# Optimization experiments

Measured on AMD Instinct MI355X. Metric: run time of the kernel, lower is better.

## Reference

```python
import jax, jax.numpy as jnp
import numpy as np

N_NODES = 100000
N_EDGES = 3200000
DIM = 64


def setup_inputs() -> dict:
    key = jax.random.key(0)
    k1, k2, k3, k4, k5, k6 = jax.random.split(key, 6)
    lap_rows = jax.random.randint(k1, (N_EDGES,), 0, N_NODES, dtype=jnp.int32)
    lap_cols = jax.random.randint(k2, (N_EDGES,), 0, N_NODES, dtype=jnp.int32)
    # normalized-Laplacian-like positive values
    lap_vals = jax.random.uniform(k3, (N_EDGES,), dtype=jnp.float32) * 0.1
    features = jax.random.normal(k4, (N_NODES, DIM), dtype=jnp.float32)
    scale = 1.0 / np.sqrt(DIM)
    W1 = jax.random.normal(k5, (DIM, DIM), dtype=jnp.float32) * scale
    b1 = jnp.zeros((DIM,), dtype=jnp.float32)
    W2 = jax.random.normal(k6, (DIM, DIM), dtype=jnp.float32) * scale
    b2 = jnp.zeros((DIM,), dtype=jnp.float32)
    return {
        "lap_rows": lap_rows, "lap_cols": lap_cols, "lap_vals": lap_vals,
        "features": features, "W1": W1, "b1": b1, "W2": W2, "b2": b2,
    }


def reference(lap_rows, lap_cols, lap_vals, features, W1, b1, W2, b2):
    # x = L @ features  (COO SpMM: gather source rows, scale, scatter-add to dest)
    msgs = lap_vals[:, None] * features[lap_cols]            # [E, D]
    x = jax.ops.segment_sum(msgs, lap_rows, num_segments=N_NODES)  # [N, D]
    # output = (L+I) E W1 + (L E * E) W2
    inter_part1 = (features + x) @ W1 + b1                   # [N, D_out]
    inter_part2 = (x * features) @ W2 + b2                   # [N, D_out]
    return inter_part1 + inter_part2
```

## Files before the change

kernel.cpp:

```cpp
#include <hip/hip_runtime.h>
#include <hip/hip_fp16.h>

#define DIM 64
#define RPB 64
#define RPB_SHIFT 6
#define SUP_SHIFT 11
#define SB_MAX 64
#define CAP 4096
#define CAPK (CAP / 1024)
#define HTILE_H 16384
#define HTILE1 8192
#define HTILE2 4096

typedef _Float16 half8 __attribute__((ext_vector_type(8)));
typedef float    f32x4 __attribute__((ext_vector_type(4)));

__global__ __launch_bounds__(256) void scatter_kernel(
    const int* __restrict__ rows, const int* __restrict__ cols,
    const float* __restrict__ vals, const float* __restrict__ feat,
    float* __restrict__ x, int E)
{
    unsigned long long t = (unsigned long long)blockIdx.x * blockDim.x + threadIdx.x;
    int e = (int)(t >> 6);
    int d = (int)(t & 63);
    if (e >= E) return;
    int r = rows[e];
    int c = cols[e];
    float v = vals[e];
    float f = feat[(size_t)c * DIM + d];
    atomicAdd(&x[(size_t)r * DIM + d], v * f);
}

__global__ __launch_bounds__(256) void cvt_kernel(
    const float* __restrict__ f, __half* __restrict__ h, int n2)
{
    int i = blockIdx.x * blockDim.x + threadIdx.x;
    if (i < n2) {
        float2 v = ((const float2*)f)[i];
        __half2 o;
        o.x = __float2half(v.x);
        o.y = __float2half(v.y);
        ((__half2*)h)[i] = o;
    }
}

__global__ __launch_bounds__(1024) void hist_kernel(
    const int* __restrict__ rows, int* __restrict__ gcnt, int E, int B)
{
    extern __shared__ int lcnt[];
    for (int i = threadIdx.x; i < B; i += 1024) lcnt[i] = 0;
    __syncthreads();
    int base = blockIdx.x * HTILE_H;
#pragma unroll
    for (int k = 0; k < HTILE_H / 1024; ++k) {
        int e = base + k * 1024 + threadIdx.x;
        if (e < E) atomicAdd(&lcnt[rows[e] >> RPB_SHIFT], 1);
    }
    __syncthreads();
    for (int i = threadIdx.x; i < B; i += 1024)
        if (lcnt[i]) atomicAdd(&gcnt[i], lcnt[i]);
}

__global__ __launch_bounds__(1024) void scan_kernel(
    const int* __restrict__ gcnt, int* __restrict__ offs, int* __restrict__ cursors,
    int* __restrict__ soffs, int* __restrict__ scursors, int B, int SB, int E)
{
    __shared__ int lds[2048];
    int t = threadIdx.x;
    int c0 = (t < B) ? gcnt[t] : 0;
    int c1 = (t + 1024 < B) ? gcnt[t + 1024] : 0;
    lds[t] = c0;
    lds[t + 1024] = c1;
    __syncthreads();
    for (int off = 1; off < 2048; off <<= 1) {
        int a = (t >= off) ? lds[t - off] : 0;
        int b = lds[t + 1024 - off];
        __syncthreads();
        lds[t] += a;
        lds[t + 1024] += b;
        __syncthreads();
    }
    if (t < B) {
        int e = lds[t] - c0;
        offs[t] = e; cursors[t] = e;
        if ((t & 31) == 0) { soffs[t >> 5] = e; scursors[t >> 5] = e; }
    }
    int t2 = t + 1024;
    if (t2 < B) {
        int e = lds[t2] - c1;
        offs[t2] = e; cursors[t2] = e;
        if ((t2 & 31) == 0) { soffs[t2 >> 5] = e; scursors[t2 >> 5] = e; }
    }
    if (t == 0) { offs[B] = E; soffs[SB] = E; }
}

__global__ __launch_bounds__(1024) void superbin_kernel(
    const int* __restrict__ rows, const int* __restrict__ cols,
    const float* __restrict__ vals, int* __restrict__ scursors,
    unsigned long long* __restrict__ sorted1, int E, int SB)
{
    __shared__ int cnt[SB_MAX];
    __shared__ int bse[SB_MAX];
    const int tid = threadIdx.x;
    if (tid < SB) cnt[tid] = 0;
    __syncthreads();
    const int tbase = blockIdx.x * HTILE1;
    int rr[HTILE1 / 1024];
#pragma unroll
    for (int k = 0; k < HTILE1 / 1024; ++k) {
        int e = tbase + k * 1024 + tid;
        rr[k] = (e < E) ? rows[e] : -1;
        if (rr[k] >= 0) atomicAdd(&cnt[rr[k] >> SUP_SHIFT], 1);
    }
    __syncthreads();
    if (tid < SB) {
        int c = cnt[tid];
        bse[tid] = c ? atomicAdd(&scursors[tid], c) : 0;
        cnt[tid] = 0;
    }
    __syncthreads();
#pragma unroll
    for (int k = 0; k < HTILE1 / 1024; ++k) {
        int e = tbase + k * 1024 + tid;
        if (rr[k] >= 0) {
            int r  = rr[k];
            int sb = r >> SUP_SHIFT;
            int slot = bse[sb] + atomicAdd(&cnt[sb], 1);
            unsigned long long pk =
                ((unsigned long long)__float_as_uint(vals[e]) << 32) |
                ((unsigned long long)(r & 2047) << 17) |
                (unsigned)cols[e];
            sorted1[slot] = pk;
        }
    }
}

__global__ __launch_bounds__(1024) void finebin_kernel(
    const unsigned long long* __restrict__ sorted1, const int* __restrict__ soffs,
    int* __restrict__ cursors, unsigned long long* __restrict__ sorted2,
    int E, int B, int SB)
{
    extern __shared__ int l[];
    int* cnt  = l;
    int* bse  = l + B;
    int* sofl = l + 2 * B;
    const int tid = threadIdx.x;
    if (tid <= SB) sofl[tid] = soffs[tid];
    for (int i = tid; i < B; i += 1024) cnt[i] = 0;
    __syncthreads();

    const int tbase = blockIdx.x * HTILE2;
    int sb0 = 0;
    {
        int lo = 0, hi = SB - 1;
        while (lo < hi) {
            int mid = (lo + hi + 1) >> 1;
            if (sofl[mid] <= tbase) lo = mid; else hi = mid - 1;
        }
        sb0 = lo;
    }

    unsigned long long pkr[HTILE2 / 1024];
    int fidr[HTILE2 / 1024];
#pragma unroll
    for (int k = 0; k < HTILE2 / 1024; ++k) {
        int i = tbase + k * 1024 + tid;
        if (i < E) {
            pkr[k] = sorted1[i];
            int sb = sb0;
            while (sofl[sb + 1] <= i) sb++;
            fidr[k] = (sb << 5) + (int)((pkr[k] >> 23) & 31);
            atomicAdd(&cnt[fidr[k]], 1);
        } else fidr[k] = -1;
    }
    __syncthreads();
    for (int i = tid; i < B; i += 1024) {
        int c = cnt[i];
        bse[i] = c ? atomicAdd(&cursors[i], c) : 0;
    }
    __syncthreads();
    for (int i = tid; i < B; i += 1024) cnt[i] = 0;
    __syncthreads();
#pragma unroll
    for (int k = 0; k < HTILE2 / 1024; ++k) {
        if (fidr[k] >= 0) {
            int f = fidr[k];
            int slot = bse[f] + atomicAdd(&cnt[f], 1);
            sorted2[slot] = pkr[k];
        }
    }
}

__global__ __launch_bounds__(1024, 8) void reduce_fused_mfma_kernel(
    const unsigned long long* __restrict__ sorted, const int* __restrict__ offs,
    const __half* __restrict__ featH,
    const float* __restrict__ W1, const float* __restrict__ b1,
    const float* __restrict__ W2, const float* __restrict__ b2,
    float* __restrict__ out, int N)
{
    __shared__ unsigned long long spk[CAP];
    __shared__ int rcnt[RPB];
    __shared__ int rbase[RPB];
    __shared__ float xs[RPB][DIM + 4];

    const int tid = threadIdx.x;
    const int b   = blockIdx.x;
    const int s    = offs[b];
    const int tend = offs[b + 1];
    int nl = tend - s;
    if (nl > CAP) nl = CAP;

    if (tid < RPB) rcnt[tid] = 0;
    __syncthreads();

    unsigned long long pkreg[CAPK];
#pragma unroll
    for (int k = 0; k < CAPK; ++k) {
        int i = k * 1024 + tid;
        pkreg[k] = (i < nl) ? sorted[s + i] : 0ull;
    }
#pragma unroll
    for (int k = 0; k < CAPK; ++k) {
        int i = k * 1024 + tid;
        if (i < nl) atomicAdd(&rcnt[(int)((pkreg[k] >> 17) & (RPB - 1))], 1);
    }
    __syncthreads();

    if (tid < 64) {
        int c = rcnt[tid];
        int v = c;
#pragma unroll
        for (int off = 1; off < 64; off <<= 1) {
            int u = __shfl_up(v, off, 64);
            if (tid >= off) v += u;
        }
        rbase[tid] = v - c;
        rcnt[tid]  = 0;
    }
    __syncthreads();

#pragma unroll
    for (int k = 0; k < CAPK; ++k) {
        int i = k * 1024 + tid;
        if (i < nl) {
            int rl  = (int)((pkreg[k] >> 17) & (RPB - 1));
            int idx = atomicAdd(&rcnt[rl], 1);
            spk[rbase[rl] + idx] = pkreg[k];
        }
    }
    __syncthreads();

    const int w    = tid >> 6;
    const int lane = tid & 63;
    const int eg   = lane >> 3;
    const int sub  = lane & 7;
    const int rowbase = b * RPB;

#pragma unroll
    for (int j = 0; j < RPB / 16; ++j) {
        int rl = w + 16 * j;
        int rs = rbase[rl];
        int rt = rs + rcnt[rl];

        __half2 hacc[4];
#pragma unroll
        for (int q = 0; q < 4; ++q) hacc[q] = __floats2half2_rn(0.f, 0.f);

        int i = rs + eg;
        for (; i + 24 < rt; i += 32) {
            unsigned long long pk0 = spk[i];
            unsigned long long pk1 = spk[i + 8];
            unsigned long long pk2 = spk[i + 16];
            unsigned long long pk3 = spk[i + 24];
            float4 rw0 = *(const float4*)(featH + (size_t)(pk0 & 0x1FFFFu) * DIM + sub * 8);
            float4 rw1 = *(const float4*)(featH + (size_t)(pk1 & 0x1FFFFu) * DIM + sub * 8);
            float4 rw2 = *(const float4*)(featH + (size_t)(pk2 & 0x1FFFFu) * DIM + sub * 8);
            float4 rw3 = *(const float4*)(featH + (size_t)(pk3 & 0x1FFFFu) * DIM + sub * 8);
            __half2 v0 = __float2half2_rn(__uint_as_float((unsigned)(pk0 >> 32)));
            __half2 v1 = __float2half2_rn(__uint_as_float((unsigned)(pk1 >> 32)));
            __half2 v2 = __float2half2_rn(__uint_as_float((unsigned)(pk2 >> 32)));
            __half2 v3 = __float2half2_rn(__uint_as_float((unsigned)(pk3 >> 32)));
            hacc[0] = __hfma2(v0, __builtin_bit_cast(__half2, rw0.x), hacc[0]);
            hacc[1] = __hfma2(v0, __builtin_bit_cast(__half2, rw0.y), hacc[1]);
            hacc[2] = __hfma2(v0, __builtin_bit_cast(__half2, rw0.z), hacc[2]);
            hacc[3] = __hfma2(v0, __builtin_bit_cast(__half2, rw0.w), hacc[3]);
            hacc[0] = __hfma2(v1, __builtin_bit_cast(__half2, rw1.x), hacc[0]);
            hacc[1] = __hfma2(v1, __builtin_bit_cast(__half2, rw1.y), hacc[1]);
            hacc[2] = __hfma2(v1, __builtin_bit_cast(__half2, rw1.z), hacc[2]);
            hacc[3] = __hfma2(v1, __builtin_bit_cast(__half2, rw1.w), hacc[3]);
            hacc[0] = __hfma2(v2, __builtin_bit_cast(__half2, rw2.x), hacc[0]);
            hacc[1] = __hfma2(v2, __builtin_bit_cast(__half2, rw2.y), hacc[1]);
            hacc[2] = __hfma2(v2, __builtin_bit_cast(__half2, rw2.z), hacc[2]);
            hacc[3] = __hfma2(v2, __builtin_bit_cast(__half2, rw2.w), hacc[3]);
            hacc[0] = __hfma2(v3, __builtin_bit_cast(__half2, rw3.x), hacc[0]);
            hacc[1] = __hfma2(v3, __builtin_bit_cast(__half2, rw3.y), hacc[1]);
            hacc[2] = __hfma2(v3, __builtin_bit_cast(__half2, rw3.z), hacc[2]);
            hacc[3] = __hfma2(v3, __builtin_bit_cast(__half2, rw3.w), hacc[3]);
        }
        for (; i < rt; i += 8) {
            unsigned long long pk0 = spk[i];
            float4 rw0 = *(const float4*)(featH + (size_t)(pk0 & 0x1FFFFu) * DIM + sub * 8);
            __half2 v0 = __float2half2_rn(__uint_as_float((unsigned)(pk0 >> 32)));
            hacc[0] = __hfma2(v0, __builtin_bit_cast(__half2, rw0.x), hacc[0]);
            hacc[1] = __hfma2(v0, __builtin_bit_cast(__half2, rw0.y), hacc[1]);
            hacc[2] = __hfma2(v0, __builtin_bit_cast(__half2, rw0.z), hacc[2]);
            hacc[3] = __hfma2(v0, __builtin_bit_cast(__half2, rw0.w), hacc[3]);
        }

        float acc[8];
#pragma unroll
        for (int q = 0; q < 4; ++q) {
            acc[2 * q]     = __low2float(hacc[q]);
            acc[2 * q + 1] = __high2float(hacc[q]);
        }
#pragma unroll
        for (int off = 8; off < 64; off <<= 1) {
#pragma unroll
            for (int q = 0; q < 8; ++q)
                acc[q] += __shfl_xor(acc[q], off, 64);
        }

        if (eg == 0) {
            float4 o; o.x = acc[0]; o.y = acc[1]; o.z = acc[2]; o.w = acc[3];
            *(float4*)&xs[rl][sub * 8] = o;
        } else if (eg == 1) {
            float4 o; o.x = acc[4]; o.y = acc[5]; o.z = acc[6]; o.w = acc[7];
            *(float4*)&xs[rl][sub * 8 + 4] = o;
        }
    }
    __syncthreads();

    if (tend - s > CAP) {
        for (int e = s + CAP + tid; e < tend; e += 1024) {
            unsigned long long pk = sorted[e];
            int rl = (int)((pk >> 17) & (RPB - 1));
            float v = __uint_as_float((unsigned)(pk >> 32));
            int c = (int)(pk & 0x1FFFFu);
            for (int d = 0; d < DIM; ++d)
                atomicAdd(&xs[rl][d], v * __half2float(featH[(size_t)c * DIM + d]));
        }
        __syncthreads();
    }

    {
        const int m    = lane & 15;
        const int quad = lane >> 4;
        const int tile = w >> 2;
        const int c    = w & 3;

        half8 wf[4];
#pragma unroll
        for (int t = 0; t < 4; ++t) {
            const float* Wsrc = (t < 2) ? W1 : W2;
            int kbase = (t & 1) * 32 + quad * 8;
            half8 wv;
#pragma unroll
            for (int j = 0; j < 8; ++j)
                wv[j] = (_Float16)Wsrc[(kbase + j) * DIM + c * 16 + m];
            wf[t] = wv;
        }
        float bias = b1[c * 16 + m] + b2[c * 16 + m];

        int rowl = tile * 16 + m;
        int grow = rowbase + rowl;
        int rldr = (grow < N) ? grow : (N - 1);
        const __half* fp = featH + (size_t)rldr * DIM + quad * 8;
        half8 flo = *(const half8*)(fp);
        half8 fhi = *(const half8*)(fp + 32);
        const float* xp = &xs[rowl][quad * 8];
        float4 xl0 = *(const float4*)(xp);
        float4 xl1 = *(const float4*)(xp + 4);
        float4 xh0 = *(const float4*)(xp + 32);
        float4 xh1 = *(const float4*)(xp + 36);

        half8 alo, ahi, blo, bhi;
        _Float16 xv;
        xv = (_Float16)xl0.x; alo[0] = flo[0] + xv; blo[0] = flo[0] * xv;
        xv = (_Float16)xl0.y; alo[1] = flo[1] + xv; blo[1] = flo[1] * xv;
        xv = (_Float16)xl0.z; alo[2] = flo[2] + xv; blo[2] = flo[2] * xv;
        xv = (_Float16)xl0.w; alo[3] = flo[3] + xv; blo[3] = flo[3] * xv;
        xv = (_Float16)xl1.x; alo[4] = flo[4] + xv; blo[4] = flo[4] * xv;
        xv = (_Float16)xl1.y; alo[5] = flo[5] + xv; blo[5] = flo[5] * xv;
        xv = (_Float16)xl1.z; alo[6] = flo[6] + xv; blo[6] = flo[6] * xv;
        xv = (_Float16)xl1.w; alo[7] = flo[7] + xv; blo[7] = flo[7] * xv;
        xv = (_Float16)xh0.x; ahi[0] = fhi[0] + xv; bhi[0] = fhi[0] * xv;
        xv = (_Float16)xh0.y; ahi[1] = fhi[1] + xv; bhi[1] = fhi[1] * xv;
        xv = (_Float16)xh0.z; ahi[2] = fhi[2] + xv; bhi[2] = fhi[2] * xv;
        xv = (_Float16)xh0.w; ahi[3] = fhi[3] + xv; bhi[3] = fhi[3] * xv;
        xv = (_Float16)xh1.x; ahi[4] = fhi[4] + xv; bhi[4] = fhi[4] * xv;
        xv = (_Float16)xh1.y; ahi[5] = fhi[5] + xv; bhi[5] = fhi[5] * xv;
        xv = (_Float16)xh1.z; ahi[6] = fhi[6] + xv; bhi[6] = fhi[6] * xv;
        xv = (_Float16)xh1.w; ahi[7] = fhi[7] + xv; bhi[7] = fhi[7] * xv;

        f32x4 a0 = { bias, bias, bias, bias };
        a0 = __builtin_amdgcn_mfma_f32_16x16x32_f16(alo, wf[0], a0, 0, 0, 0);
        a0 = __builtin_amdgcn_mfma_f32_16x16x32_f16(ahi, wf[1], a0, 0, 0, 0);
        a0 = __builtin_amdgcn_mfma_f32_16x16x32_f16(blo, wf[2], a0, 0, 0, 0);
        a0 = __builtin_amdgcn_mfma_f32_16x16x32_f16(bhi, wf[3], a0, 0, 0, 0);

#pragma unroll
        for (int reg = 0; reg < 4; ++reg) {
            int orow = rowbase + tile * 16 + quad * 4 + reg;
            if (orow < N)
                out[(size_t)orow * DIM + c * 16 + m] = a0[reg];
        }
    }
}

__global__ __launch_bounds__(256) void transform_mfma_kernel(
    const __half* __restrict__ featH, const float* __restrict__ x,
    const float* __restrict__ W1, const float* __restrict__ b1,
    const float* __restrict__ W2, const float* __restrict__ b2,
    float* __restrict__ out, int N)
{
    const int lane = threadIdx.x & 63;
    const int m    = lane & 15;
    const int quad = lane >> 4;

    half8 wfrag[4][4];
#pragma unroll
    for (int t = 0; t < 4; ++t) {
        const float* Wsrc = (t < 2) ? W1 : W2;
        int kbase = (t & 1) * 32 + quad * 8;
#pragma unroll
        for (int c = 0; c < 4; ++c) {
            int col = c * 16 + m;
            half8 w;
#pragma unroll
            for (int j = 0; j < 8; ++j)
                w[j] = (_Float16)Wsrc[(kbase + j) * DIM + col];
            wfrag[t][c] = w;
        }
    }
    float bias[4];
#pragma unroll
    for (int c = 0; c < 4; ++c)
        bias[c] = b1[c * 16 + m] + b2[c * 16 + m];

    const int ntiles = (N + 15) / 16;
    const int wid    = (int)((blockIdx.x * blockDim.x + threadIdx.x) >> 6);
    const int nwaves = (int)((gridDim.x * blockDim.x) >> 6);

    for (int tile = wid; tile < ntiles; tile += nwaves) {
        int row  = tile * 16 + m;
        int rldr = (row < N) ? row : (N - 1);
        const __half* fp = featH + (size_t)rldr * DIM + quad * 8;
        const float*  xp = x     + (size_t)rldr * DIM + quad * 8;
        half8 flo = *(const half8*)(fp);
        half8 fhi = *(const half8*)(fp + 32);
        float4 xl0 = *(const float4*)(xp);
        float4 xl1 = *(const float4*)(xp + 4);
        float4 xh0 = *(const float4*)(xp + 32);
        float4 xh1 = *(const float4*)(xp + 36);

        half8 alo, ahi, blo, bhi;
        _Float16 xv;
        xv = (_Float16)xl0.x; alo[0] = flo[0] + xv; blo[0] = flo[0] * xv;
        xv = (_Float16)xl0.y; alo[1] = flo[1] + xv; blo[1] = flo[1] * xv;
        xv = (_Float16)xl0.z; alo[2] = flo[2] + xv; blo[2] = flo[2] * xv;
        xv = (_Float16)xl0.w; alo[3] = flo[3] + xv; blo[3] = flo[3] * xv;
        xv = (_Float16)xl1.x; alo[4] = flo[4] + xv; blo[4] = flo[4] * xv;
        xv = (_Float16)xl1.y; alo[5] = flo[5] + xv; blo[5] = flo[5] * xv;
        xv = (_Float16)xl1.z; alo[6] = flo[6] + xv; blo[6] = flo[6] * xv;
        xv = (_Float16)xl1.w; alo[7] = flo[7] + xv; blo[7] = flo[7] * xv;
        xv = (_Float16)xh0.x; ahi[0] = fhi[0] + xv; bhi[0] = fhi[0] * xv;
        xv = (_Float16)xh0.y; ahi[1] = fhi[1] + xv; bhi[1] = fhi[1] * xv;
        xv = (_Float16)xh0.z; ahi[2] = fhi[2] + xv; bhi[2] = fhi[2] * xv;
        xv = (_Float16)xh0.w; ahi[3] = fhi[3] + xv; bhi[3] = fhi[3] * xv;
        xv = (_Float16)xh1.x; ahi[4] = fhi[4] + xv; bhi[4] = fhi[4] * xv;
        xv = (_Float16)xh1.y; ahi[5] = fhi[5] + xv; bhi[5] = fhi[5] * xv;
        xv = (_Float16)xh1.z; ahi[6] = fhi[6] + xv; bhi[6] = fhi[6] * xv;
        xv = (_Float16)xh1.w; ahi[7] = fhi[7] + xv; bhi[7] = fhi[7] * xv;

        f32x4 acc[4];
#pragma unroll
        for (int c = 0; c < 4; ++c) {
            f32x4 a0 = { bias[c], bias[c], bias[c], bias[c] };
            a0 = __builtin_amdgcn_mfma_f32_16x16x32_f16(alo, wfrag[0][c], a0, 0, 0, 0);
            a0 = __builtin_amdgcn_mfma_f32_16x16x32_f16(ahi, wfrag[1][c], a0, 0, 0, 0);
            a0 = __builtin_amdgcn_mfma_f32_16x16x32_f16(blo, wfrag[2][c], a0, 0, 0, 0);
            a0 = __builtin_amdgcn_mfma_f32_16x16x32_f16(bhi, wfrag[3][c], a0, 0, 0, 0);
            acc[c] = a0;
        }

#pragma unroll
        for (int reg = 0; reg < 4; ++reg) {
            int orow = tile * 16 + quad * 4 + reg;
            if (orow < N) {
#pragma unroll
                for (int c = 0; c < 4; ++c)
                    out[(size_t)orow * DIM + c * 16 + m] = acc[c][reg];
            }
        }
    }
}

extern "C" void kernel_launch(void* const* d_in, const int* in_sizes, int n_in,
                              void* d_out, int out_size, void* d_ws, size_t ws_size,
                              hipStream_t stream)
{
    const int*   rows = (const int*)d_in[0];
    const int*   cols = (const int*)d_in[1];
    const float* vals = (const float*)d_in[2];
    const float* feat = (const float*)d_in[3];
    const float* W1   = (const float*)d_in[4];
    const float* b1   = (const float*)d_in[5];
    const float* W2   = (const float*)d_in[6];
    const float* b2   = (const float*)d_in[7];
    float* out = (float*)d_out;

    const int E  = in_sizes[0];
    const int N  = in_sizes[3] / DIM;
    const int B  = (N + RPB - 1) / RPB;
    const int SB = (B + 31) / 32;

    char* ws = (char*)d_ws;
    size_t xBytes     = (size_t)N * DIM * sizeof(float);
    size_t hBytes     = (((size_t)N * DIM * sizeof(__half)) + 255) / 256 * 256;
    size_t offsBytes  = (((size_t)(B + 1) * sizeof(int)) + 255) / 256 * 256;
    size_t cursBytes  = (((size_t)B * sizeof(int)) + 255) / 256 * 256;
    size_t soffBytes  = (((size_t)(SB + 1) * sizeof(int)) + 255) / 256 * 256;
    size_t scurBytes  = (((size_t)SB * sizeof(int)) + 255) / 256 * 256;
    size_t sortBytes  = (size_t)E * 8;

    float*              x        = (float*)ws;
    __half*             featH    = (__half*)(ws + xBytes);
    int*                offs     = (int*)(ws + xBytes + hBytes);
    int*                cursors  = (int*)(ws + xBytes + hBytes + offsBytes);
    int*                soffs    = (int*)(ws + xBytes + hBytes + offsBytes + cursBytes);
    int*                scursors = (int*)(ws + xBytes + hBytes + offsBytes + cursBytes + soffBytes);
    unsigned long long* sorted1  = (unsigned long long*)(ws + xBytes + hBytes + offsBytes +
                                                         cursBytes + soffBytes + scurBytes);
    unsigned long long* sorted2  = sorted1 + E;
    size_t need = xBytes + hBytes + offsBytes + cursBytes + soffBytes + scurBytes + 2 * sortBytes;

    cvt_kernel<<<(N * DIM / 2 + 255) / 256, 256, 0, stream>>>(feat, featH, N * DIM / 2);

    if (ws_size >= need && B <= 2048 && SB <= SB_MAX && N <= 131072) {
        const int NTH = (E + HTILE_H - 1) / HTILE_H;
        const int NT1 = (E + HTILE1 - 1) / HTILE1;
        const int NT2 = (E + HTILE2 - 1) / HTILE2;
        hipMemsetAsync(offs, 0, (size_t)(B + 1) * sizeof(int), stream);
        hist_kernel<<<NTH, 1024, (size_t)B * 4, stream>>>(rows, offs, E, B);
        scan_kernel<<<1, 1024, 0, stream>>>(offs, offs, cursors, soffs, scursors, B, SB, E);
        superbin_kernel<<<NT1, 1024, 0, stream>>>(rows, cols, vals, scursors, sorted1, E, SB);
        finebin_kernel<<<NT2, 1024, (size_t)(2 * B + SB + 1) * 4, stream>>>(
            sorted1, soffs, cursors, sorted2, E, B, SB);
        reduce_fused_mfma_kernel<<<B, 1024, 0, stream>>>(sorted2, offs, featH,
                                                         W1, b1, W2, b2, out, N);
    } else {
        hipMemsetAsync(x, 0, xBytes, stream);
        unsigned long long threads = (unsigned long long)E * DIM;
        unsigned int blocks = (unsigned int)((threads + 255ull) / 256ull);
        scatter_kernel<<<blocks, 256, 0, stream>>>(rows, cols, vals, feat, x, E);
        transform_mfma_kernel<<<640, 256, 0, stream>>>(featH, x, W1, b1, W2, b2, out, N);
    }
}
```

Measured before the change: 250.6 us.

## Gather FP8-quantized features in SpMM reduce and fuse conversion with histogram

The fp16 feature conversion is merged with the row histogram into one prep kernel, which also writes an FP8 copy of the features. The reduce kernel now gathers 8-byte FP8 rows instead of 16-byte fp16 rows for the neighbour aggregation, halving the random-gather bytes. The weight-fragment loads are hoisted to the start of the reduce kernel so they overlap the sort-load phase. The FP8 path costs precision in the aggregated features, which risks failing the accuracy tolerance, and adds unpack instructions per gathered element.

```diff
diff --git a/kernel.cpp b/kernel.cpp
--- a/kernel.cpp
+++ b/kernel.cpp
@@ -14,6 +14,14 @@
 
 typedef _Float16 half8 __attribute__((ext_vector_type(8)));
 typedef float    f32x4 __attribute__((ext_vector_type(4)));
+typedef float    f32x2 __attribute__((ext_vector_type(2)));
+
+template <bool HI>
+__device__ __forceinline__ __half2 q2h(unsigned int w)
+{
+    f32x2 f = __builtin_amdgcn_cvt_pk_f32_fp8(w, HI);
+    return __floats2half2_rn(f[0], f[1]);
+}
 
 __global__ __launch_bounds__(256) void scatter_kernel(
     const int* __restrict__ rows, const int* __restrict__ cols,
@@ -44,21 +52,48 @@
     }
 }
 
-__global__ __launch_bounds__(1024) void hist_kernel(
-    const int* __restrict__ rows, int* __restrict__ gcnt, int E, int B)
-{
-    extern __shared__ int lcnt[];
-    for (int i = threadIdx.x; i < B; i += 1024) lcnt[i] = 0;
-    __syncthreads();
-    int base = blockIdx.x * HTILE_H;
-#pragma unroll
-    for (int k = 0; k < HTILE_H / 1024; ++k) {
-        int e = base + k * 1024 + threadIdx.x;
-        if (e < E) atomicAdd(&lcnt[rows[e] >> RPB_SHIFT], 1);
-    }
-    __syncthreads();
-    for (int i = threadIdx.x; i < B; i += 1024)
-        if (lcnt[i]) atomicAdd(&gcnt[i], lcnt[i]);
+__global__ __launch_bounds__(1024) void prep_kernel(
+    const float* __restrict__ feat, __half* __restrict__ featH,
+    unsigned char* __restrict__ featQ,
+    const int* __restrict__ rows, int* __restrict__ gcnt,
+    int n8, int NC, int E, int B)
+{
+    if ((int)blockIdx.x < NC) {
+        int i = blockIdx.x * 1024 + threadIdx.x;
+        if (i < n8) {
+            const float4* src = (const float4*)(feat + (size_t)i * 8);
+            float4 a = src[0], b = src[1];
+            __half2 h0 = __floats2half2_rn(a.x, a.y);
+            __half2 h1 = __floats2half2_rn(a.z, a.w);
+            __half2 h2 = __floats2half2_rn(b.x, b.y);
+            __half2 h3 = __floats2half2_rn(b.z, b.w);
+            float4 ho;
+            ho.x = __builtin_bit_cast(float, h0);
+            ho.y = __builtin_bit_cast(float, h1);
+            ho.z = __builtin_bit_cast(float, h2);
+            ho.w = __builtin_bit_cast(float, h3);
+            *(float4*)(featH + (size_t)i * 8) = ho;
+            unsigned int q0 = __builtin_amdgcn_cvt_pk_fp8_f32(a.x, a.y, 0, false);
+            q0 = __builtin_amdgcn_cvt_pk_fp8_f32(a.z, a.w, (int)q0, true);
+            unsigned int q1 = __builtin_amdgcn_cvt_pk_fp8_f32(b.x, b.y, 0, false);
+            q1 = __builtin_amdgcn_cvt_pk_fp8_f32(b.z, b.w, (int)q1, true);
+            uint2 qo; qo.x = q0; qo.y = q1;
+            *(uint2*)(featQ + (size_t)i * 8) = qo;
+        }
+    } else {
+        extern __shared__ int lcnt[];
+        for (int i = threadIdx.x; i < B; i += 1024) lcnt[i] = 0;
+        __syncthreads();
+        int base = ((int)blockIdx.x - NC) * HTILE_H;
+#pragma unroll
+        for (int k = 0; k < HTILE_H / 1024; ++k) {
+            int e = base + k * 1024 + threadIdx.x;
+            if (e < E) atomicAdd(&lcnt[rows[e] >> RPB_SHIFT], 1);
+        }
+        __syncthreads();
+        for (int i = threadIdx.x; i < B; i += 1024)
+            if (lcnt[i]) atomicAdd(&gcnt[i], lcnt[i]);
+    }
 }
 
 __global__ __launch_bounds__(1024) void scan_kernel(
@@ -193,7 +228,7 @@
 
 __global__ __launch_bounds__(1024, 8) void reduce_fused_mfma_kernel(
     const unsigned long long* __restrict__ sorted, const int* __restrict__ offs,
-    const __half* __restrict__ featH,
+    const unsigned char* __restrict__ featQ, const __half* __restrict__ featH,
     const float* __restrict__ W1, const float* __restrict__ b1,
     const float* __restrict__ W2, const float* __restrict__ b2,
     float* __restrict__ out, int N)
@@ -205,6 +240,28 @@
 
     const int tid = threadIdx.x;
     const int b   = blockIdx.x;
+    const int w    = tid >> 6;
+    const int lane = tid & 63;
+
+    half8 wf[4];
+    float bias;
+    {
+        const int m    = lane & 15;
+        const int quad = lane >> 4;
+        const int cw   = w & 3;
+#pragma unroll
+        for (int t = 0; t < 4; ++t) {
+            const float* Wsrc = (t < 2) ? W1 : W2;
+            int kbase = (t & 1) * 32 + quad * 8;
+            half8 wv;
+#pragma unroll
+            for (int j = 0; j < 8; ++j)
+                wv[j] = (_Float16)Wsrc[(kbase + j) * DIM + cw * 16 + m];
+            wf[t] = wv;
+        }
+        bias = b1[cw * 16 + m] + b2[cw * 16 + m];
+    }
+
     const int s    = offs[b];
     const int tend = offs[b + 1];
     int nl = tend - s;
@@ -250,8 +307,6 @@
     }
     __syncthreads();
 
-    const int w    = tid >> 6;
-    const int lane = tid & 63;
     const int eg   = lane >> 3;
     const int sub  = lane & 7;
     const int rowbase = b * RPB;
@@ -272,39 +327,39 @@
             unsigned long long pk1 = spk[i + 8];
             unsigned long long pk2 = spk[i + 16];
             unsigned long long pk3 = spk[i + 24];
-            float4 rw0 = *(const float4*)(featH + (size_t)(pk0 & 0x1FFFFu) * DIM + sub * 8);
-            float4 rw1 = *(const float4*)(featH + (size_t)(pk1 & 0x1FFFFu) * DIM + sub * 8);
-            float4 rw2 = *(const float4*)(featH + (size_t)(pk2 & 0x1FFFFu) * DIM + sub * 8);
-            float4 rw3 = *(const float4*)(featH + (size_t)(pk3 & 0x1FFFFu) * DIM + sub * 8);
+            uint2 q0 = *(const uint2*)(featQ + ((size_t)(pk0 & 0x1FFFFu) << 6) + sub * 8);
+            uint2 q1 = *(const uint2*)(featQ + ((size_t)(pk1 & 0x1FFFFu) << 6) + sub * 8);
+            uint2 q2 = *(const uint2*)(featQ + ((size_t)(pk2 & 0x1FFFFu) << 6) + sub * 8);
+            uint2 q3 = *(const uint2*)(featQ + ((size_t)(pk3 & 0x1FFFFu) << 6) + sub * 8);
             __half2 v0 = __float2half2_rn(__uint_as_float((unsigned)(pk0 >> 32)));
             __half2 v1 = __float2half2_rn(__uint_as_float((unsigned)(pk1 >> 32)));
             __half2 v2 = __float2half2_rn(__uint_as_float((unsigned)(pk2 >> 32)));
             __half2 v3 = __float2half2_rn(__uint_as_float((unsigned)(pk3 >> 32)));
-            hacc[0] = __hfma2(v0, __builtin_bit_cast(__half2, rw0.x), hacc[0]);
-            hacc[1] = __hfma2(v0, __builtin_bit_cast(__half2, rw0.y), hacc[1]);
-            hacc[2] = __hfma2(v0, __builtin_bit_cast(__half2, rw0.z), hacc[2]);
-            hacc[3] = __hfma2(v0, __builtin_bit_cast(__half2, rw0.w), hacc[3]);
-            hacc[0] = __hfma2(v1, __builtin_bit_cast(__half2, rw1.x), hacc[0]);
-            hacc[1] = __hfma2(v1, __builtin_bit_cast(__half2, rw1.y), hacc[1]);
-            hacc[2] = __hfma2(v1, __builtin_bit_cast(__half2, rw1.z), hacc[2]);
-            hacc[3] = __hfma2(v1, __builtin_bit_cast(__half2, rw1.w), hacc[3]);
-            hacc[0] = __hfma2(v2, __builtin_bit_cast(__half2, rw2.x), hacc[0]);
-            hacc[1] = __hfma2(v2, __builtin_bit_cast(__half2, rw2.y), hacc[1]);
-            hacc[2] = __hfma2(v2, __builtin_bit_cast(__half2, rw2.z), hacc[2]);
-            hacc[3] = __hfma2(v2, __builtin_bit_cast(__half2, rw2.w), hacc[3]);
-            hacc[0] = __hfma2(v3, __builtin_bit_cast(__half2, rw3.x), hacc[0]);
-            hacc[1] = __hfma2(v3, __builtin_bit_cast(__half2, rw3.y), hacc[1]);
-            hacc[2] = __hfma2(v3, __builtin_bit_cast(__half2, rw3.z), hacc[2]);
-            hacc[3] = __hfma2(v3, __builtin_bit_cast(__half2, rw3.w), hacc[3]);
+            hacc[0] = __hfma2(v0, q2h<false>(q0.x), hacc[0]);
+            hacc[1] = __hfma2(v0, q2h<true >(q0.x), hacc[1]);
+            hacc[2] = __hfma2(v0, q2h<false>(q0.y), hacc[2]);
+            hacc[3] = __hfma2(v0, q2h<true >(q0.y), hacc[3]);
+            hacc[0] = __hfma2(v1, q2h<false>(q1.x), hacc[0]);
+            hacc[1] = __hfma2(v1, q2h<true >(q1.x), hacc[1]);
+            hacc[2] = __hfma2(v1, q2h<false>(q1.y), hacc[2]);
+            hacc[3] = __hfma2(v1, q2h<true >(q1.y), hacc[3]);
+            hacc[0] = __hfma2(v2, q2h<false>(q2.x), hacc[0]);
+            hacc[1] = __hfma2(v2, q2h<true >(q2.x), hacc[1]);
+            hacc[2] = __hfma2(v2, q2h<false>(q2.y), hacc[2]);
+            hacc[3] = __hfma2(v2, q2h<true >(q2.y), hacc[3]);
+            hacc[0] = __hfma2(v3, q2h<false>(q3.x), hacc[0]);
+            hacc[1] = __hfma2(v3, q2h<true >(q3.x), hacc[1]);
+            hacc[2] = __hfma2(v3, q2h<false>(q3.y), hacc[2]);
+            hacc[3] = __hfma2(v3, q2h<true >(q3.y), hacc[3]);
         }
         for (; i < rt; i += 8) {
             unsigned long long pk0 = spk[i];
-            float4 rw0 = *(const float4*)(featH + (size_t)(pk0 & 0x1FFFFu) * DIM + sub * 8);
+            uint2 q0 = *(const uint2*)(featQ + ((size_t)(pk0 & 0x1FFFFu) << 6) + sub * 8);
             __half2 v0 = __float2half2_rn(__uint_as_float((unsigned)(pk0 >> 32)));
-            hacc[0] = __hfma2(v0, __builtin_bit_cast(__half2, rw0.x), hacc[0]);
-            hacc[1] = __hfma2(v0, __builtin_bit_cast(__half2, rw0.y), hacc[1]);
-            hacc[2] = __hfma2(v0, __builtin_bit_cast(__half2, rw0.z), hacc[2]);
-            hacc[3] = __hfma2(v0, __builtin_bit_cast(__half2, rw0.w), hacc[3]);
+            hacc[0] = __hfma2(v0, q2h<false>(q0.x), hacc[0]);
+            hacc[1] = __hfma2(v0, q2h<true >(q0.x), hacc[1]);
+            hacc[2] = __hfma2(v0, q2h<false>(q0.y), hacc[2]);
+            hacc[3] = __hfma2(v0, q2h<true >(q0.y), hacc[3]);
         }
 
         float acc[8];
@@ -346,20 +401,6 @@
         const int m    = lane & 15;
         const int quad = lane >> 4;
         const int tile = w >> 2;
-        const int c    = w & 3;
-
-        half8 wf[4];
-#pragma unroll
-        for (int t = 0; t < 4; ++t) {
-            const float* Wsrc = (t < 2) ? W1 : W2;
-            int kbase = (t & 1) * 32 + quad * 8;
-            half8 wv;
-#pragma unroll
-            for (int j = 0; j < 8; ++j)
-                wv[j] = (_Float16)Wsrc[(kbase + j) * DIM + c * 16 + m];
-            wf[t] = wv;
-        }
-        float bias = b1[c * 16 + m] + b2[c * 16 + m];
 
         int rowl = tile * 16 + m;
         int grow = rowbase + rowl;
@@ -398,11 +439,12 @@
         a0 = __builtin_amdgcn_mfma_f32_16x16x32_f16(blo, wf[2], a0, 0, 0, 0);
         a0 = __builtin_amdgcn_mfma_f32_16x16x32_f16(bhi, wf[3], a0, 0, 0, 0);
 
+        const int cw = w & 3;
 #pragma unroll
         for (int reg = 0; reg < 4; ++reg) {
             int orow = rowbase + tile * 16 + quad * 4 + reg;
             if (orow < N)
-                out[(size_t)orow * DIM + c * 16 + m] = a0[reg];
+                out[(size_t)orow * DIM + cw * 16 + m] = a0[reg];
         }
     }
 }
@@ -517,6 +559,7 @@
     char* ws = (char*)d_ws;
     size_t xBytes     = (size_t)N * DIM * sizeof(float);
     size_t hBytes     = (((size_t)N * DIM * sizeof(__half)) + 255) / 256 * 256;
+    size_t qBytes     = (((size_t)N * DIM) + 255) / 256 * 256;
     size_t offsBytes  = (((size_t)(B + 1) * sizeof(int)) + 255) / 256 * 256;
     size_t cursBytes  = (((size_t)B * sizeof(int)) + 255) / 256 * 256;
     size_t soffBytes  = (((size_t)(SB + 1) * sizeof(int)) + 255) / 256 * 256;
@@ -525,30 +568,33 @@
 
     float*              x        = (float*)ws;
     __half*             featH    = (__half*)(ws + xBytes);
-    int*                offs     = (int*)(ws + xBytes + hBytes);
-    int*                cursors  = (int*)(ws + xBytes + hBytes + offsBytes);
-    int*                soffs    = (int*)(ws + xBytes + hBytes + offsBytes + cursBytes);
-    int*                scursors = (int*)(ws + xBytes + hBytes + offsBytes + cursBytes + soffBytes);
-    unsigned long long* sorted1  = (unsigned long long*)(ws + xBytes + hBytes + offsBytes +
+    unsigned char*      featQ    = (unsigned char*)(ws + xBytes + hBytes);
+    int*                offs     = (int*)(ws + xBytes + hBytes + qBytes);
+    int*                cursors  = (int*)(ws + xBytes + hBytes + qBytes + offsBytes);
+    int*                soffs    = (int*)(ws + xBytes + hBytes + qBytes + offsBytes + cursBytes);
+    int*                scursors = (int*)(ws + xBytes + hBytes + qBytes + offsBytes + cursBytes + soffBytes);
+    unsigned long long* sorted1  = (unsigned long long*)(ws + xBytes + hBytes + qBytes + offsBytes +
                                                          cursBytes + soffBytes + scurBytes);
     unsigned long long* sorted2  = sorted1 + E;
-    size_t need = xBytes + hBytes + offsBytes + cursBytes + soffBytes + scurBytes + 2 * sortBytes;
-
-    cvt_kernel<<<(N * DIM / 2 + 255) / 256, 256, 0, stream>>>(feat, featH, N * DIM / 2);
+    size_t need = xBytes + hBytes + qBytes + offsBytes + cursBytes + soffBytes + scurBytes + 2 * sortBytes;
 
     if (ws_size >= need && B <= 2048 && SB <= SB_MAX && N <= 131072) {
+        const int n8  = N * DIM / 8;
+        const int NC  = (n8 + 1023) / 1024;
         const int NTH = (E + HTILE_H - 1) / HTILE_H;
         const int NT1 = (E + HTILE1 - 1) / HTILE1;
         const int NT2 = (E + HTILE2 - 1) / HTILE2;
         hipMemsetAsync(offs, 0, (size_t)(B + 1) * sizeof(int), stream);
-        hist_kernel<<<NTH, 1024, (size_t)B * 4, stream>>>(rows, offs, E, B);
+        prep_kernel<<<NC + NTH, 1024, (size_t)B * 4, stream>>>(
+            feat, featH, featQ, rows, offs, n8, NC, E, B);
         scan_kernel<<<1, 1024, 0, stream>>>(offs, offs, cursors, soffs, scursors, B, SB, E);
         superbin_kernel<<<NT1, 1024, 0, stream>>>(rows, cols, vals, scursors, sorted1, E, SB);
         finebin_kernel<<<NT2, 1024, (size_t)(2 * B + SB + 1) * 4, stream>>>(
             sorted1, soffs, cursors, sorted2, E, B, SB);
-        reduce_fused_mfma_kernel<<<B, 1024, 0, stream>>>(sorted2, offs, featH,
+        reduce_fused_mfma_kernel<<<B, 1024, 0, stream>>>(sorted2, offs, featQ, featH,
                                                          W1, b1, W2, b2, out, N);
     } else {
+        cvt_kernel<<<(N * DIM / 2 + 255) / 256, 256, 0, stream>>>(feat, featH, N * DIM / 2);
         hipMemsetAsync(x, 0, xBytes, stream);
         unsigned long long threads = (unsigned long long)E * DIM;
         unsigned int blocks = (unsigned int)((threads + 255ull) / 256ull);
```

New measurement: 264.4 us. 1.05x slower.
